# Optimization experiments

Measured on AMD Instinct MI355X. Metric: run time of the kernel, lower is better.

The kernel has to match this reference:

```python
import jax, jax.numpy as jnp
import numpy as np

B, T, D, E, V = 16, 256, 512, 512, 32000  # batch, seqlen, embed_dim, encoder_embed_dim, vocab


def setup_inputs() -> dict:
    key = jax.random.key(0)
    ks = jax.random.split(key, 13)
    s = 0.05
    return {
        "prev_output_tokens": jax.random.randint(ks[0], (B, T), 0, V),
        "encoder_out": jax.random.normal(ks[1], (B, E), jnp.float32),
        "embed": jax.random.normal(ks[2], (V, D), jnp.float32) * s,
        "W_ih0": jax.random.normal(ks[3], (4 * D, E + D), jnp.float32) * s,
        "W_hh0": jax.random.normal(ks[4], (4 * D, D), jnp.float32) * s,
        "b_ih0": jax.random.normal(ks[5], (4 * D,), jnp.float32) * s,
        "b_hh0": jax.random.normal(ks[6], (4 * D,), jnp.float32) * s,
        "W_ih1": jax.random.normal(ks[7], (4 * D, D), jnp.float32) * s,
        "W_hh1": jax.random.normal(ks[8], (4 * D, D), jnp.float32) * s,
        "b_ih1": jax.random.normal(ks[9], (4 * D,), jnp.float32) * s,
        "b_hh1": jax.random.normal(ks[10], (4 * D,), jnp.float32) * s,
        "W_out": jax.random.normal(ks[11], (V, D), jnp.float32) * s,
        "b_out": jax.random.normal(ks[12], (V,), jnp.float32) * s,
    }


def _lstm_cell(x, h, c, W_ih, W_hh, b_ih, b_hh):
    # torch.nn.LSTMCell gate order: i, f, g, o
    gates = x @ W_ih.T + b_ih + h @ W_hh.T + b_hh
    i, f, g, o = jnp.split(gates, 4, axis=-1)
    c_new = jax.nn.sigmoid(f) * c + jax.nn.sigmoid(i) * jnp.tanh(g)
    h_new = jax.nn.sigmoid(o) * jnp.tanh(c_new)
    return h_new, c_new


def reference(prev_output_tokens, encoder_out, embed, W_ih0, W_hh0, b_ih0, b_hh0,
              W_ih1, W_hh1, b_ih1, b_hh1, W_out, b_out):
    # padding_idx=0 -> row 0 of the embedding table is zero
    embed = embed.at[0].set(0.0)
    x = embed[prev_output_tokens]          # [B, T, D]  (dropout: eval mode -> identity)
    x = jnp.swapaxes(x, 0, 1)              # [T, B, D]
    bsz = x.shape[1]
    h0 = jnp.zeros((bsz, W_hh0.shape[1]), x.dtype)
    c0, h1, c1 = h0, h0, h0

    def step(carry, x_t):
        h0, c0, h1, c1 = carry
        inp = jnp.concatenate([x_t, encoder_out], axis=1)   # [B, D+E]
        h0, c0 = _lstm_cell(inp, h0, c0, W_ih0, W_hh0, b_ih0, b_hh0)
        h1, c1 = _lstm_cell(h0, h1, c1, W_ih1, W_hh1, b_ih1, b_hh1)
        return (h0, c0, h1, c1), h1

    _, outs = jax.lax.scan(step, (h0, c0, h1, c1), x)       # outs: [T, B, D]
    outs = jnp.swapaxes(outs, 0, 1)                          # [B, T, D]
    return outs @ W_out.T + b_out                            # [B, T, V]
```

## Files before the change

### kernel.cpp

```cpp
#include <hip/hip_runtime.h>
#include <hip/hip_bf16.h>
#include <math.h>

#define BB 16
#define TT 256
#define DD 512
#define EE 512
#define VV 32000
#define G4 2048

typedef __attribute__((ext_vector_type(4))) float f32x4;
typedef __attribute__((ext_vector_type(8))) short bf16x8;
typedef __attribute__((ext_vector_type(4))) unsigned u32x4;

union lf_u { u32x4 q; bf16x8 v; };

#define SENTMASK32 0x40004000u

__device__ __forceinline__ unsigned short f2bf(float x) {
    unsigned u = __float_as_uint(x);
    unsigned r = (u + 0x7FFFu + ((u >> 16) & 1u)) >> 16;
    return (unsigned short)r;
}

__device__ __forceinline__ float sigmoidf_(float x) { return 1.0f / (1.0f + expf(-x)); }

__global__ __launch_bounds__(256) void k_gather(const int* __restrict__ tok,
        const float* __restrict__ embed, unsigned short* __restrict__ Xb) {
    int m = blockIdx.x;
    int tk = tok[m];
    const float* src = embed + (size_t)tk * DD;
    int i = threadIdx.x * 2;
    float vx = 0.f, vy = 0.f;
    if (tk != 0) { float2 v = *(const float2*)&src[i]; vx = v.x; vy = v.y; }
    ushort2 o; o.x = f2bf(vx); o.y = f2bf(vy);
    *(ushort2*)&Xb[(size_t)m * DD + i] = o;
}

__global__ __launch_bounds__(256) void k_cvt(const float* __restrict__ in,
        unsigned short* __restrict__ out, int n4) {
    int i = blockIdx.x * 256 + threadIdx.x;
    if (i >= n4) return;
    float4 v = ((const float4*)in)[i];
    ushort4 o; o.x = f2bf(v.x); o.y = f2bf(v.y); o.z = f2bf(v.z); o.w = f2bf(v.w);
    ((ushort4*)out)[i] = o;
}

__global__ __launch_bounds__(256) void k_cvt_wih0x(const float* __restrict__ Wih0,
        unsigned short* __restrict__ out) {
    int i = blockIdx.x * 256 + threadIdx.x;
    int j = i >> 7;
    int k4 = (i & 127) << 2;
    float4 v = *(const float4*)&Wih0[(size_t)j * (EE + DD) + k4];
    ushort4 o; o.x = f2bf(v.x); o.y = f2bf(v.y); o.z = f2bf(v.z); o.w = f2bf(v.w);
    *(ushort4*)&out[(size_t)j * DD + k4] = o;
}

__global__ __launch_bounds__(256) void k_encterm(const float* __restrict__ enc,
        const float* __restrict__ Wih0, const float* __restrict__ bih0,
        const float* __restrict__ bhh0, float* __restrict__ et) {
    int b = blockIdx.x >> 3, jc = blockIdx.x & 7;
    int tid = threadIdx.x, lane = tid & 63, w = tid >> 6;
    __shared__ float es[EE];
    if (tid < EE / 4) *(float4*)&es[tid * 4] = *(const float4*)&enc[b * EE + tid * 4];
    __syncthreads();
    float4 e0 = *(const float4*)&es[lane * 4];
    float4 e1 = *(const float4*)&es[256 + lane * 4];
    for (int o = 0; o < 64; ++o) {
        int j = jc * 256 + w * 64 + o;
        const float4* Wr = (const float4*)&Wih0[(size_t)j * (EE + DD) + DD];
        float4 w0 = Wr[lane], w1 = Wr[64 + lane];
        float s = w0.x*e0.x + w0.y*e0.y + w0.z*e0.z + w0.w*e0.w
                + w1.x*e1.x + w1.y*e1.y + w1.z*e1.z + w1.w*e1.w;
        #pragma unroll
        for (int off = 32; off; off >>= 1) s += __shfl_xor(s, off);
        if (lane == 0) et[b * G4 + j] = s + bih0[j] + bhh0[j];
    }
}

template<int EPI>
__global__ __launch_bounds__(256) void k_gemm_bt(
        const unsigned short* __restrict__ A, const unsigned short* __restrict__ Bm,
        float* __restrict__ C, const float* __restrict__ extra,
        int M, int N, int K) {
    __shared__ __align__(16) unsigned short Alds[128 * 32];
    __shared__ __align__(16) unsigned short Blds[128 * 32];
    int tid = threadIdx.x, lane = tid & 63, w = tid >> 6;
    int wr = w >> 1, wc = w & 1;
    int nwgx = gridDim.x;
    int nwg = nwgx * gridDim.y;
    int lin = blockIdx.y * nwgx + blockIdx.x;
    int cpx = nwg >> 3;
    lin = (lin & 7) * cpx + (lin >> 3);
    int m0 = (lin % nwgx) * 128, n0 = (lin / nwgx) * 128;
    f32x4 acc[4][4];
    #pragma unroll
    for (int i = 0; i < 4; i++)
        #pragma unroll
        for (int j = 0; j < 4; j++) acc[i][j] = (f32x4)0.f;

    const char* Abase = (const char*)A;
    const char* Bbase = (const char*)Bm;
    for (int ks = 0; ks < K; ks += 32) {
        #pragma unroll
        for (int c = 0; c < 2; ++c) {
            int f = (tid + c * 256) * 16;
            int row = f >> 6;
            int inb = f & 63;
            const char* gA = Abase + (((size_t)(m0 + row) * K + ks) * 2 + inb);
            __builtin_amdgcn_global_load_lds(
                (const __attribute__((address_space(1))) void*)gA,
                (__attribute__((address_space(3))) void*)((char*)Alds + f), 16, 0, 0);
            const char* gB = Bbase + (((size_t)(n0 + row) * K + ks) * 2 + inb);
            __builtin_amdgcn_global_load_lds(
                (const __attribute__((address_space(1))) void*)gB,
                (__attribute__((address_space(3))) void*)((char*)Blds + f), 16, 0, 0);
        }
        __syncthreads();
        bf16x8 af[4], bfr[4];
        int r = lane & 15, ko = (lane >> 4) * 8;
        #pragma unroll
        for (int mi = 0; mi < 4; ++mi)
            af[mi] = *(const bf16x8*)&Alds[(wr * 64 + mi * 16 + r) * 32 + ko];
        #pragma unroll
        for (int ni = 0; ni < 4; ++ni)
            bfr[ni] = *(const bf16x8*)&Blds[(wc * 64 + ni * 16 + r) * 32 + ko];
        #pragma unroll
        for (int mi = 0; mi < 4; ++mi)
            #pragma unroll
            for (int ni = 0; ni < 4; ++ni)
                acc[mi][ni] = __builtin_amdgcn_mfma_f32_16x16x32_bf16(af[mi], bfr[ni], acc[mi][ni], 0, 0, 0);
        __syncthreads();
    }
    int cr = (lane >> 4) * 4, cc = lane & 15;
    #pragma unroll
    for (int mi = 0; mi < 4; ++mi) {
        #pragma unroll
        for (int ni = 0; ni < 4; ++ni) {
            int col = n0 + wc * 64 + ni * 16 + cc;
            #pragma unroll
            for (int rr = 0; rr < 4; ++rr) {
                int rowg = m0 + wr * 64 + mi * 16 + cr + rr;
                float v = acc[mi][ni][rr];
                if (EPI == 0) v += extra[(rowg >> 8) * G4 + col];
                else          v += extra[col];
                C[(size_t)rowg * N + col] = v;
            }
        }
    }
}

__device__ __forceinline__ void load16sc(const void* base, lf_u* o) {
    asm volatile(
        "global_load_dwordx4 %0, %16, off sc0 sc1\n\t"
        "global_load_dwordx4 %1, %16, off offset:64 sc0 sc1\n\t"
        "global_load_dwordx4 %2, %16, off offset:128 sc0 sc1\n\t"
        "global_load_dwordx4 %3, %16, off offset:192 sc0 sc1\n\t"
        "global_load_dwordx4 %4, %16, off offset:256 sc0 sc1\n\t"
        "global_load_dwordx4 %5, %16, off offset:320 sc0 sc1\n\t"
        "global_load_dwordx4 %6, %16, off offset:384 sc0 sc1\n\t"
        "global_load_dwordx4 %7, %16, off offset:448 sc0 sc1\n\t"
        "global_load_dwordx4 %8, %16, off offset:512 sc0 sc1\n\t"
        "global_load_dwordx4 %9, %16, off offset:576 sc0 sc1\n\t"
        "global_load_dwordx4 %10, %16, off offset:640 sc0 sc1\n\t"
        "global_load_dwordx4 %11, %16, off offset:704 sc0 sc1\n\t"
        "global_load_dwordx4 %12, %16, off offset:768 sc0 sc1\n\t"
        "global_load_dwordx4 %13, %16, off offset:832 sc0 sc1\n\t"
        "global_load_dwordx4 %14, %16, off offset:896 sc0 sc1\n\t"
        "global_load_dwordx4 %15, %16, off offset:960 sc0 sc1\n\t"
        "s_waitcnt vmcnt(0)"
        : "=&v"(o[0].q), "=&v"(o[1].q), "=&v"(o[2].q), "=&v"(o[3].q),
          "=&v"(o[4].q), "=&v"(o[5].q), "=&v"(o[6].q), "=&v"(o[7].q),
          "=&v"(o[8].q), "=&v"(o[9].q), "=&v"(o[10].q), "=&v"(o[11].q),
          "=&v"(o[12].q), "=&v"(o[13].q), "=&v"(o[14].q), "=&v"(o[15].q)
        : "v"(base)
        : "memory");
}

__device__ __forceinline__ void poll16sc(const void* base, lf_u* o) {
    for (;;) {
        load16sc(base, o);
        unsigned bad = 0;
        #pragma unroll
        for (int kt = 0; kt < 16; ++kt)
            bad |= (o[kt].q.x | o[kt].q.y | o[kt].q.z | o[kt].q.w);
        if (!__any((bad & SENTMASK32) != 0)) return;
    }
}

__device__ __forceinline__ void store8sc(void* addr, unsigned long long v) {
    asm volatile("global_store_dwordx2 %0, %1, off sc0 sc1"
                 :: "v"(addr), "v"(v) : "memory");
}

__global__ __launch_bounds__(64) void k_recur(
        const float* __restrict__ Gx,
        const float* __restrict__ Whh0,
        const float* __restrict__ Wih1, const float* __restrict__ Whh1,
        const float* __restrict__ bih1, const float* __restrict__ bhh1,
        unsigned short* h0hist, unsigned short* outsb,
        const unsigned short* zbuf) {
    __shared__ __align__(16) unsigned short wfrag[4 * 32 * 512];
    __shared__ __align__(8)  unsigned short houts[16 * 16];
    const int l = threadIdx.x;
    const int bid = blockIdx.x;
    const int role = bid >> 5;
    const int blk = bid & 31;
    const int d0 = blk * 16;
    const int r16 = l & 15;
    const int q = l >> 4;
    const int ksub = q * 8;
    const int b0 = q * 4;
    const int srow = l >> 2;
    const int sseg = l & 3;

    const int nkt = role ? 32 : 16;
    for (int tile = 0; tile < 4; ++tile) {
        int j = tile * 512 + d0 + r16;
        for (int kt = 0; kt < nkt; ++kt) {
            const float* src;
            if (role == 0)    src = Whh0 + (size_t)j * DD + kt * 32 + ksub;
            else if (kt < 16) src = Wih1 + (size_t)j * DD + kt * 32 + ksub;
            else              src = Whh1 + (size_t)j * DD + (kt - 16) * 32 + ksub;
            float4 x = *(const float4*)src;
            float4 y = *(const float4*)(src + 4);
            bf16x8 w;
            w[0] = f2bf(x.x); w[1] = f2bf(x.y); w[2] = f2bf(x.z); w[3] = f2bf(x.w);
            w[4] = f2bf(y.x); w[5] = f2bf(y.y); w[6] = f2bf(y.z); w[7] = f2bf(y.w);
            *(bf16x8*)&wfrag[((tile * 32 + kt) * 64 + l) * 8] = w;
        }
    }
    __syncthreads();

    float cst[4] = {0.f, 0.f, 0.f, 0.f};
    lf_u xf[16];

    if (role == 0) {
        for (int t = 0; t < TT; ++t) {
            float gx[4][4];
            #pragma unroll
            for (int ni = 0; ni < 4; ++ni)
                #pragma unroll
                for (int rr = 0; rr < 4; ++rr)
                    gx[ni][rr] = Gx[((size_t)(b0 + rr) * TT + t) * G4 + ni * 512 + d0 + r16];

            const char* xb = (const char*)(h0hist + (size_t)t * (BB * DD) + r16 * DD) + q * 16;
            poll16sc(xb, xf);

            f32x4 acc[4];
            #pragma unroll
            for (int ni = 0; ni < 4; ++ni) acc[ni] = (f32x4)0.f;
            #pragma unroll
            for (int kt = 0; kt < 16; ++kt) {
                #pragma unroll
                for (int ni = 0; ni < 4; ++ni) {
                    bf16x8 wf = *(const bf16x8*)&wfrag[((ni * 32 + kt) * 64 + l) * 8];
                    acc[ni] = __builtin_amdgcn_mfma_f32_16x16x32_bf16(xf[kt].v, wf, acc[ni], 0, 0, 0);
                }
            }
            #pragma unroll
            for (int rr = 0; rr < 4; ++rr) {
                float gi = acc[0][rr] + gx[0][rr], gf = acc[1][rr] + gx[1][rr];
                float gg = acc[2][rr] + gx[2][rr], go = acc[3][rr] + gx[3][rr];
                float cn = sigmoidf_(gf) * cst[rr] + sigmoidf_(gi) * tanhf(gg);
                float hn = sigmoidf_(go) * tanhf(cn);
                cst[rr] = cn;
                houts[(b0 + rr) * 16 + r16] = f2bf(hn);
            }
            asm volatile("" ::: "memory");
            {
                const unsigned short* hp = &houts[srow * 16 + sseg * 4];
                unsigned long long w8 =  (unsigned long long)hp[0]
                                      | ((unsigned long long)hp[1] << 16)
                                      | ((unsigned long long)hp[2] << 32)
                                      | ((unsigned long long)hp[3] << 48);
                store8sc(h0hist + (size_t)(t + 1) * (BB * DD) + srow * DD + d0 + sseg * 4, w8);
            }
        }
    } else {
        lf_u hf[16];
        float bin[4];
        #pragma unroll
        for (int ni = 0; ni < 4; ++ni)
            bin[ni] = bih1[ni * 512 + d0 + r16] + bhh1[ni * 512 + d0 + r16];
        for (int t = 0; t < TT; ++t) {
            const char* xb = (const char*)(h0hist + (size_t)(t + 1) * (BB * DD) + r16 * DD) + q * 16;
            poll16sc(xb, xf);

            f32x4 acc[4];
            #pragma unroll
            for (int ni = 0; ni < 4; ++ni)
                acc[ni] = (f32x4){bin[ni], bin[ni], bin[ni], bin[ni]};
            #pragma unroll
            for (int kt = 0; kt < 16; ++kt) {
                #pragma unroll
                for (int ni = 0; ni < 4; ++ni) {
                    bf16x8 wf = *(const bf16x8*)&wfrag[((ni * 32 + kt) * 64 + l) * 8];
                    acc[ni] = __builtin_amdgcn_mfma_f32_16x16x32_bf16(xf[kt].v, wf, acc[ni], 0, 0, 0);
                }
            }
            const char* hb = (t == 0)
                ? (const char*)(zbuf + r16 * DD) + q * 16
                : (const char*)(outsb + ((size_t)r16 * TT + (t - 1)) * DD) + q * 16;
            poll16sc(hb, hf);
            #pragma unroll
            for (int kt = 0; kt < 16; ++kt) {
                #pragma unroll
                for (int ni = 0; ni < 4; ++ni) {
                    bf16x8 wf = *(const bf16x8*)&wfrag[((ni * 32 + 16 + kt) * 64 + l) * 8];
                    acc[ni] = __builtin_amdgcn_mfma_f32_16x16x32_bf16(hf[kt].v, wf, acc[ni], 0, 0, 0);
                }
            }
            #pragma unroll
            for (int rr = 0; rr < 4; ++rr) {
                float gi = acc[0][rr], gf = acc[1][rr], gg = acc[2][rr], go = acc[3][rr];
                float cn = sigmoidf_(gf) * cst[rr] + sigmoidf_(gi) * tanhf(gg);
                float hn = sigmoidf_(go) * tanhf(cn);
                cst[rr] = cn;
                houts[(b0 + rr) * 16 + r16] = f2bf(hn);
            }
            asm volatile("" ::: "memory");
            {
                const unsigned short* hp = &houts[srow * 16 + sseg * 4];
                unsigned long long w8 =  (unsigned long long)hp[0]
                                      | ((unsigned long long)hp[1] << 16)
                                      | ((unsigned long long)hp[2] << 32)
                                      | ((unsigned long long)hp[3] << 48);
                store8sc(outsb + ((size_t)srow * TT + t) * DD + d0 + sseg * 4, w8);
            }
        }
    }
}

extern "C" void kernel_launch(void* const* d_in, const int* in_sizes, int n_in,
                              void* d_out, int out_size, void* d_ws, size_t ws_size,
                              hipStream_t stream) {
    const int*   tok   = (const int*)  d_in[0];
    const float* enc   = (const float*)d_in[1];
    const float* embed = (const float*)d_in[2];
    const float* Wih0  = (const float*)d_in[3];
    const float* Whh0  = (const float*)d_in[4];
    const float* bih0  = (const float*)d_in[5];
    const float* bhh0  = (const float*)d_in[6];
    const float* Wih1  = (const float*)d_in[7];
    const float* Whh1  = (const float*)d_in[8];
    const float* bih1  = (const float*)d_in[9];
    const float* bhh1  = (const float*)d_in[10];
    const float* Wout  = (const float*)d_in[11];
    const float* bout  = (const float*)d_in[12];
    float* out = (float*)d_out;

    char* ws = (char*)d_ws;
    size_t off = 0;
    auto alloc = [&](size_t bytes) -> char* {
        char* p = ws + off; off += (bytes + 255) & ~(size_t)255; return p;
    };
    unsigned short* Xb     = (unsigned short*)alloc((size_t)BB * TT * DD * 2);
    unsigned short* Wih0xb = (unsigned short*)alloc((size_t)G4 * DD * 2);
    unsigned short* Woutb  = (unsigned short*)alloc((size_t)VV * DD * 2);
    float*          et     = (float*)alloc((size_t)BB * G4 * sizeof(float));
    float*          Gx     = (float*)alloc((size_t)BB * TT * G4 * sizeof(float));
    unsigned short* outsb  = (unsigned short*)alloc((size_t)BB * TT * DD * 2);
    unsigned short* h0hist = (unsigned short*)alloc((size_t)(TT + 1) * BB * DD * 2);
    unsigned short* zbuf   = (unsigned short*)alloc((size_t)BB * DD * 2);

    hipMemsetAsync(h0hist, 0, (size_t)BB * DD * 2, stream);
    hipMemsetAsync(h0hist + (size_t)BB * DD, 0xFF, (size_t)TT * BB * DD * 2, stream);
    hipMemsetAsync(outsb, 0xFF, (size_t)BB * TT * DD * 2, stream);
    hipMemsetAsync(zbuf, 0, (size_t)BB * DD * 2, stream);

    k_gather<<<BB * TT, 256, 0, stream>>>(tok, embed, Xb);
    k_cvt<<<(VV * DD / 4 + 255) / 256, 256, 0, stream>>>(Wout, Woutb, VV * DD / 4);
    k_cvt_wih0x<<<(G4 * DD / 4) / 256, 256, 0, stream>>>(Wih0, Wih0xb);
    k_encterm<<<BB * 8, 256, 0, stream>>>(enc, Wih0, bih0, bhh0, et);

    dim3 g1(BB * TT / 128, G4 / 128);
    k_gemm_bt<0><<<g1, 256, 0, stream>>>(Xb, Wih0xb, Gx, et, BB * TT, G4, DD);

    k_recur<<<64, 64, 0, stream>>>(Gx, Whh0, Wih1, Whh1, bih1, bhh1,
                                   h0hist, outsb, zbuf);

    dim3 g2(BB * TT / 128, VV / 128);
    k_gemm_bt<1><<<g2, 256, 0, stream>>>(outsb, Woutb, out, bout, BB * TT, VV, DD);
}
```

Before: 1.677 ms.

## Fuse recurrence and output projection into one persistent kernel with overlap

Merges the LSTM recurrence kernel and the vocab projection GEMM into a single persistent kernel. 64 blocks run the recurrence and publish per-block progress counters after every timestep. The remaining 192 blocks take output GEMM tiles (16 timesteps by 8 batches by 128 vocab columns) from an atomic ticket and spin until the recurrence has produced those timesteps. This overlaps the large projection GEMM with the serial recurrence, at the cost of competing for memory bandwidth, extra polling traffic, and a GEMM tile layout with strided rows.

```diff
diff --git a/kernel.cpp b/kernel.cpp
--- a/kernel.cpp
+++ b/kernel.cpp
@@ -8,6 +8,7 @@
 #define EE 512
 #define VV 32000
 #define G4 2048
+#define NTILES (16 * 2 * 250)
 
 typedef __attribute__((ext_vector_type(4))) float f32x4;
 typedef __attribute__((ext_vector_type(8))) short bf16x8;
@@ -78,8 +79,7 @@
     }
 }
 
-template<int EPI>
-__global__ __launch_bounds__(256) void k_gemm_bt(
+__global__ __launch_bounds__(256) void k_gemm0(
         const unsigned short* __restrict__ A, const unsigned short* __restrict__ Bm,
         float* __restrict__ C, const float* __restrict__ extra,
         int M, int N, int K) {
@@ -141,10 +141,7 @@
             #pragma unroll
             for (int rr = 0; rr < 4; ++rr) {
                 int rowg = m0 + wr * 64 + mi * 16 + cr + rr;
-                float v = acc[mi][ni][rr];
-                if (EPI == 0) v += extra[(rowg >> 8) * G4 + col];
-                else          v += extra[col];
-                C[(size_t)rowg * N + col] = v;
+                C[(size_t)rowg * N + col] = acc[mi][ni][rr] + extra[(rowg >> 8) * G4 + col];
             }
         }
     }
@@ -193,140 +190,242 @@
                  :: "v"(addr), "v"(v) : "memory");
 }
 
-__global__ __launch_bounds__(64) void k_recur(
+__global__ __launch_bounds__(256) void k_mega(
         const float* __restrict__ Gx,
         const float* __restrict__ Whh0,
         const float* __restrict__ Wih1, const float* __restrict__ Whh1,
         const float* __restrict__ bih1, const float* __restrict__ bhh1,
         unsigned short* h0hist, unsigned short* outsb,
-        const unsigned short* zbuf) {
-    __shared__ __align__(16) unsigned short wfrag[4 * 32 * 512];
-    __shared__ __align__(8)  unsigned short houts[16 * 16];
-    const int l = threadIdx.x;
+        const unsigned short* zbuf,
+        const unsigned short* __restrict__ Woutb, const float* __restrict__ bout,
+        float* __restrict__ out,
+        int* ep1, int* tick) {
+    __shared__ __align__(16) unsigned char smem[4 * 32 * 512 * 2 + 512];
+    __shared__ int idSh;
     const int bid = blockIdx.x;
-    const int role = bid >> 5;
-    const int blk = bid & 31;
-    const int d0 = blk * 16;
-    const int r16 = l & 15;
-    const int q = l >> 4;
-    const int ksub = q * 8;
-    const int b0 = q * 4;
-    const int srow = l >> 2;
-    const int sseg = l & 3;
-
-    const int nkt = role ? 32 : 16;
-    for (int tile = 0; tile < 4; ++tile) {
-        int j = tile * 512 + d0 + r16;
-        for (int kt = 0; kt < nkt; ++kt) {
-            const float* src;
-            if (role == 0)    src = Whh0 + (size_t)j * DD + kt * 32 + ksub;
-            else if (kt < 16) src = Wih1 + (size_t)j * DD + kt * 32 + ksub;
-            else              src = Whh1 + (size_t)j * DD + (kt - 16) * 32 + ksub;
-            float4 x = *(const float4*)src;
-            float4 y = *(const float4*)(src + 4);
-            bf16x8 w;
-            w[0] = f2bf(x.x); w[1] = f2bf(x.y); w[2] = f2bf(x.z); w[3] = f2bf(x.w);
-            w[4] = f2bf(y.x); w[5] = f2bf(y.y); w[6] = f2bf(y.z); w[7] = f2bf(y.w);
-            *(bf16x8*)&wfrag[((tile * 32 + kt) * 64 + l) * 8] = w;
+
+    if (bid < 64) {
+        unsigned short* wfrag = (unsigned short*)smem;
+        unsigned short* houts = (unsigned short*)(smem + 4 * 32 * 512 * 2);
+        const int l = threadIdx.x;
+        const int role = bid >> 5;
+        const int blk = bid & 31;
+        const int d0 = blk * 16;
+        const int r16 = l & 15;
+        const int q = (l >> 4) & 3;
+        const int ksub = q * 8;
+        const int b0 = q * 4;
+        const int srow = (l >> 2) & 15;
+        const int sseg = l & 3;
+
+        const int nkt = role ? 32 : 16;
+        if (l < 64) {
+            for (int tile = 0; tile < 4; ++tile) {
+                int j = tile * 512 + d0 + r16;
+                for (int kt = 0; kt < nkt; ++kt) {
+                    const float* src;
+                    if (role == 0)    src = Whh0 + (size_t)j * DD + kt * 32 + ksub;
+                    else if (kt < 16) src = Wih1 + (size_t)j * DD + kt * 32 + ksub;
+                    else              src = Whh1 + (size_t)j * DD + (kt - 16) * 32 + ksub;
+                    float4 x = *(const float4*)src;
+                    float4 y = *(const float4*)(src + 4);
+                    bf16x8 w;
+                    w[0] = f2bf(x.x); w[1] = f2bf(x.y); w[2] = f2bf(x.z); w[3] = f2bf(x.w);
+                    w[4] = f2bf(y.x); w[5] = f2bf(y.y); w[6] = f2bf(y.z); w[7] = f2bf(y.w);
+                    *(bf16x8*)&wfrag[((tile * 32 + kt) * 64 + l) * 8] = w;
+                }
+            }
         }
-    }
-    __syncthreads();
-
-    float cst[4] = {0.f, 0.f, 0.f, 0.f};
-    lf_u xf[16];
-
-    if (role == 0) {
-        for (int t = 0; t < TT; ++t) {
-            float gx[4][4];
+        __syncthreads();
+        if (l >= 64) return;
+
+        float cst[4] = {0.f, 0.f, 0.f, 0.f};
+        lf_u xf[16];
+
+        if (role == 0) {
+            for (int t = 0; t < TT; ++t) {
+                float gx[4][4];
+                #pragma unroll
+                for (int ni = 0; ni < 4; ++ni)
+                    #pragma unroll
+                    for (int rr = 0; rr < 4; ++rr)
+                        gx[ni][rr] = Gx[((size_t)(b0 + rr) * TT + t) * G4 + ni * 512 + d0 + r16];
+
+                const char* xb = (const char*)(h0hist + (size_t)t * (BB * DD) + r16 * DD) + q * 16;
+                poll16sc(xb, xf);
+
+                f32x4 acc[4];
+                #pragma unroll
+                for (int ni = 0; ni < 4; ++ni) acc[ni] = (f32x4)0.f;
+                #pragma unroll
+                for (int kt = 0; kt < 16; ++kt) {
+                    #pragma unroll
+                    for (int ni = 0; ni < 4; ++ni) {
+                        bf16x8 wf = *(const bf16x8*)&wfrag[((ni * 32 + kt) * 64 + l) * 8];
+                        acc[ni] = __builtin_amdgcn_mfma_f32_16x16x32_bf16(xf[kt].v, wf, acc[ni], 0, 0, 0);
+                    }
+                }
+                #pragma unroll
+                for (int rr = 0; rr < 4; ++rr) {
+                    float gi = acc[0][rr] + gx[0][rr], gf = acc[1][rr] + gx[1][rr];
+                    float gg = acc[2][rr] + gx[2][rr], go = acc[3][rr] + gx[3][rr];
+                    float cn = sigmoidf_(gf) * cst[rr] + sigmoidf_(gi) * tanhf(gg);
+                    float hn = sigmoidf_(go) * tanhf(cn);
+                    cst[rr] = cn;
+                    houts[(b0 + rr) * 16 + r16] = f2bf(hn);
+                }
+                asm volatile("" ::: "memory");
+                {
+                    const unsigned short* hp = &houts[srow * 16 + sseg * 4];
+                    unsigned long long w8 =  (unsigned long long)hp[0]
+                                          | ((unsigned long long)hp[1] << 16)
+                                          | ((unsigned long long)hp[2] << 32)
+                                          | ((unsigned long long)hp[3] << 48);
+                    store8sc(h0hist + (size_t)(t + 1) * (BB * DD) + srow * DD + d0 + sseg * 4, w8);
+                }
+            }
+        } else {
+            lf_u hf[16];
+            float bin[4];
             #pragma unroll
             for (int ni = 0; ni < 4; ++ni)
-                #pragma unroll
-                for (int rr = 0; rr < 4; ++rr)
-                    gx[ni][rr] = Gx[((size_t)(b0 + rr) * TT + t) * G4 + ni * 512 + d0 + r16];
-
-            const char* xb = (const char*)(h0hist + (size_t)t * (BB * DD) + r16 * DD) + q * 16;
-            poll16sc(xb, xf);
-
-            f32x4 acc[4];
-            #pragma unroll
-            for (int ni = 0; ni < 4; ++ni) acc[ni] = (f32x4)0.f;
-            #pragma unroll
-            for (int kt = 0; kt < 16; ++kt) {
-                #pragma unroll
-                for (int ni = 0; ni < 4; ++ni) {
-                    bf16x8 wf = *(const bf16x8*)&wfrag[((ni * 32 + kt) * 64 + l) * 8];
-                    acc[ni] = __builtin_amdgcn_mfma_f32_16x16x32_bf16(xf[kt].v, wf, acc[ni], 0, 0, 0);
-                }
-            }
-            #pragma unroll
-            for (int rr = 0; rr < 4; ++rr) {
-                float gi = acc[0][rr] + gx[0][rr], gf = acc[1][rr] + gx[1][rr];
-                float gg = acc[2][rr] + gx[2][rr], go = acc[3][rr] + gx[3][rr];
-                float cn = sigmoidf_(gf) * cst[rr] + sigmoidf_(gi) * tanhf(gg);
-                float hn = sigmoidf_(go) * tanhf(cn);
-                cst[rr] = cn;
-                houts[(b0 + rr) * 16 + r16] = f2bf(hn);
-            }
-            asm volatile("" ::: "memory");
-            {
-                const unsigned short* hp = &houts[srow * 16 + sseg * 4];
-                unsigned long long w8 =  (unsigned long long)hp[0]
-                                      | ((unsigned long long)hp[1] << 16)
-                                      | ((unsigned long long)hp[2] << 32)
-                                      | ((unsigned long long)hp[3] << 48);
-                store8sc(h0hist + (size_t)(t + 1) * (BB * DD) + srow * DD + d0 + sseg * 4, w8);
+                bin[ni] = bih1[ni * 512 + d0 + r16] + bhh1[ni * 512 + d0 + r16];
+            for (int t = 0; t < TT; ++t) {
+                const char* xb = (const char*)(h0hist + (size_t)(t + 1) * (BB * DD) + r16 * DD) + q * 16;
+                poll16sc(xb, xf);
+
+                f32x4 acc[4];
+                #pragma unroll
+                for (int ni = 0; ni < 4; ++ni)
+                    acc[ni] = (f32x4){bin[ni], bin[ni], bin[ni], bin[ni]};
+                #pragma unroll
+                for (int kt = 0; kt < 16; ++kt) {
+                    #pragma unroll
+                    for (int ni = 0; ni < 4; ++ni) {
+                        bf16x8 wf = *(const bf16x8*)&wfrag[((ni * 32 + kt) * 64 + l) * 8];
+                        acc[ni] = __builtin_amdgcn_mfma_f32_16x16x32_bf16(xf[kt].v, wf, acc[ni], 0, 0, 0);
+                    }
+                }
+                const char* hb = (t == 0)
+                    ? (const char*)(zbuf + r16 * DD) + q * 16
+                    : (const char*)(outsb + ((size_t)r16 * TT + (t - 1)) * DD) + q * 16;
+                poll16sc(hb, hf);
+                #pragma unroll
+                for (int kt = 0; kt < 16; ++kt) {
+                    #pragma unroll
+                    for (int ni = 0; ni < 4; ++ni) {
+                        bf16x8 wf = *(const bf16x8*)&wfrag[((ni * 32 + 16 + kt) * 64 + l) * 8];
+                        acc[ni] = __builtin_amdgcn_mfma_f32_16x16x32_bf16(hf[kt].v, wf, acc[ni], 0, 0, 0);
+                    }
+                }
+                #pragma unroll
+                for (int rr = 0; rr < 4; ++rr) {
+                    float gi = acc[0][rr], gf = acc[1][rr], gg = acc[2][rr], go = acc[3][rr];
+                    float cn = sigmoidf_(gf) * cst[rr] + sigmoidf_(gi) * tanhf(gg);
+                    float hn = sigmoidf_(go) * tanhf(cn);
+                    cst[rr] = cn;
+                    houts[(b0 + rr) * 16 + r16] = f2bf(hn);
+                }
+                asm volatile("" ::: "memory");
+                {
+                    const unsigned short* hp = &houts[srow * 16 + sseg * 4];
+                    unsigned long long w8 =  (unsigned long long)hp[0]
+                                          | ((unsigned long long)hp[1] << 16)
+                                          | ((unsigned long long)hp[2] << 32)
+                                          | ((unsigned long long)hp[3] << 48);
+                    store8sc(outsb + ((size_t)srow * TT + t) * DD + d0 + sseg * 4, w8);
+                }
+                asm volatile("s_waitcnt vmcnt(0)" ::: "memory");
+                if (l == 0) {
+                    int tv = t + 1;
+                    asm volatile("global_store_dword %0, %1, off sc0 sc1"
+                                 :: "v"(ep1 + blk * 16), "v"(tv) : "memory");
+                }
             }
         }
     } else {
-        lf_u hf[16];
-        float bin[4];
-        #pragma unroll
-        for (int ni = 0; ni < 4; ++ni)
-            bin[ni] = bih1[ni * 512 + d0 + r16] + bhh1[ni * 512 + d0 + r16];
-        for (int t = 0; t < TT; ++t) {
-            const char* xb = (const char*)(h0hist + (size_t)(t + 1) * (BB * DD) + r16 * DD) + q * 16;
-            poll16sc(xb, xf);
-
-            f32x4 acc[4];
+        unsigned short* Alds = (unsigned short*)smem;
+        unsigned short* Blds = (unsigned short*)(smem + 8192);
+        const int tid = threadIdx.x, lane = tid & 63, w = tid >> 6;
+        const int wr = w >> 1, wc = w & 1;
+
+        for (;;) {
+            if (tid == 0) idSh = atomicAdd(tick, 1);
+            __syncthreads();
+            int id = idSh;
+            if (id >= NTILES) break;
+
+            int chunk = id / 500;
+            int rem   = id % 500;
+            int bg    = rem / 250;
+            int nt    = rem % 250;
+            int t0 = chunk * 16;
+            int n0 = nt * 128;
+            int target = t0 + 16;
+
+            for (;;) {
+                int v;
+                asm volatile("global_load_dword %0, %1, off sc0 sc1\n\ts_waitcnt vmcnt(0)"
+                             : "=v"(v) : "v"(ep1 + (lane & 31) * 16) : "memory");
+                if (__all(v >= target)) break;
+                __builtin_amdgcn_s_sleep(4);
+            }
+
+            f32x4 acc[4][4];
             #pragma unroll
-            for (int ni = 0; ni < 4; ++ni)
-                acc[ni] = (f32x4){bin[ni], bin[ni], bin[ni], bin[ni]};
+            for (int i = 0; i < 4; i++)
+                #pragma unroll
+                for (int j = 0; j < 4; j++) acc[i][j] = (f32x4)0.f;
+
+            for (int ks = 0; ks < DD; ks += 32) {
+                #pragma unroll
+                for (int c = 0; c < 2; ++c) {
+                    int f = (tid + c * 256) * 16;
+                    int row = f >> 6;
+                    int inb = f & 63;
+                    int bb = bg * 8 + (row >> 4);
+                    int tt = t0 + (row & 15);
+                    const char* gA = (const char*)outsb +
+                        (((size_t)bb * TT + tt) * DD + ks) * 2 + inb;
+                    __builtin_amdgcn_global_load_lds(
+                        (const __attribute__((address_space(1))) void*)gA,
+                        (__attribute__((address_space(3))) void*)((char*)Alds + f), 16, 0, 0);
+                    const char* gB = (const char*)Woutb +
+                        (((size_t)(n0 + row)) * DD + ks) * 2 + inb;
+                    __builtin_amdgcn_global_load_lds(
+                        (const __attribute__((address_space(1))) void*)gB,
+                        (__attribute__((address_space(3))) void*)((char*)Blds + f), 16, 0, 0);
+                }
+                __syncthreads();
+                bf16x8 af[4], bfr[4];
+                int r = lane & 15, ko = (lane >> 4) * 8;
+                #pragma unroll
+                for (int mi = 0; mi < 4; ++mi)
+                    af[mi] = *(const bf16x8*)&Alds[(wr * 64 + mi * 16 + r) * 32 + ko];
+                #pragma unroll
+                for (int ni = 0; ni < 4; ++ni)
+                    bfr[ni] = *(const bf16x8*)&Blds[(wc * 64 + ni * 16 + r) * 32 + ko];
+                #pragma unroll
+                for (int mi = 0; mi < 4; ++mi)
+                    #pragma unroll
+                    for (int ni = 0; ni < 4; ++ni)
+                        acc[mi][ni] = __builtin_amdgcn_mfma_f32_16x16x32_bf16(af[mi], bfr[ni], acc[mi][ni], 0, 0, 0);
+                __syncthreads();
+            }
+            int cr = (lane >> 4) * 4, cc = lane & 15;
             #pragma unroll
-            for (int kt = 0; kt < 16; ++kt) {
+            for (int mi = 0; mi < 4; ++mi) {
                 #pragma unroll
                 for (int ni = 0; ni < 4; ++ni) {
-                    bf16x8 wf = *(const bf16x8*)&wfrag[((ni * 32 + kt) * 64 + l) * 8];
-                    acc[ni] = __builtin_amdgcn_mfma_f32_16x16x32_bf16(xf[kt].v, wf, acc[ni], 0, 0, 0);
-                }
-            }
-            const char* hb = (t == 0)
-                ? (const char*)(zbuf + r16 * DD) + q * 16
-                : (const char*)(outsb + ((size_t)r16 * TT + (t - 1)) * DD) + q * 16;
-            poll16sc(hb, hf);
-            #pragma unroll
-            for (int kt = 0; kt < 16; ++kt) {
-                #pragma unroll
-                for (int ni = 0; ni < 4; ++ni) {
-                    bf16x8 wf = *(const bf16x8*)&wfrag[((ni * 32 + 16 + kt) * 64 + l) * 8];
-                    acc[ni] = __builtin_amdgcn_mfma_f32_16x16x32_bf16(hf[kt].v, wf, acc[ni], 0, 0, 0);
-                }
-            }
-            #pragma unroll
-            for (int rr = 0; rr < 4; ++rr) {
-                float gi = acc[0][rr], gf = acc[1][rr], gg = acc[2][rr], go = acc[3][rr];
-                float cn = sigmoidf_(gf) * cst[rr] + sigmoidf_(gi) * tanhf(gg);
-                float hn = sigmoidf_(go) * tanhf(cn);
-                cst[rr] = cn;
-                houts[(b0 + rr) * 16 + r16] = f2bf(hn);
-            }
-            asm volatile("" ::: "memory");
-            {
-                const unsigned short* hp = &houts[srow * 16 + sseg * 4];
-                unsigned long long w8 =  (unsigned long long)hp[0]
-                                      | ((unsigned long long)hp[1] << 16)
-                                      | ((unsigned long long)hp[2] << 32)
-                                      | ((unsigned long long)hp[3] << 48);
-                store8sc(outsb + ((size_t)srow * TT + t) * DD + d0 + sseg * 4, w8);
+                    int col = n0 + wc * 64 + ni * 16 + cc;
+                    #pragma unroll
+                    for (int rr = 0; rr < 4; ++rr) {
+                        int rloc = wr * 64 + mi * 16 + cr + rr;
+                        int bb = bg * 8 + (rloc >> 4);
+                        int tt = t0 + (rloc & 15);
+                        out[((size_t)bb * TT + tt) * VV + col] = acc[mi][ni][rr] + bout[col];
+                    }
+                }
             }
         }
     }
@@ -363,11 +462,15 @@
     unsigned short* outsb  = (unsigned short*)alloc((size_t)BB * TT * DD * 2);
     unsigned short* h0hist = (unsigned short*)alloc((size_t)(TT + 1) * BB * DD * 2);
     unsigned short* zbuf   = (unsigned short*)alloc((size_t)BB * DD * 2);
+    int*            ep1    = (int*)alloc(32 * 16 * sizeof(int));
+    int*            tick   = (int*)alloc(64 * sizeof(int));
 
     hipMemsetAsync(h0hist, 0, (size_t)BB * DD * 2, stream);
     hipMemsetAsync(h0hist + (size_t)BB * DD, 0xFF, (size_t)TT * BB * DD * 2, stream);
     hipMemsetAsync(outsb, 0xFF, (size_t)BB * TT * DD * 2, stream);
     hipMemsetAsync(zbuf, 0, (size_t)BB * DD * 2, stream);
+    hipMemsetAsync(ep1, 0, 32 * 16 * sizeof(int), stream);
+    hipMemsetAsync(tick, 0, 64 * sizeof(int), stream);
 
     k_gather<<<BB * TT, 256, 0, stream>>>(tok, embed, Xb);
     k_cvt<<<(VV * DD / 4 + 255) / 256, 256, 0, stream>>>(Wout, Woutb, VV * DD / 4);
@@ -375,11 +478,9 @@
     k_encterm<<<BB * 8, 256, 0, stream>>>(enc, Wih0, bih0, bhh0, et);
 
     dim3 g1(BB * TT / 128, G4 / 128);
-    k_gemm_bt<0><<<g1, 256, 0, stream>>>(Xb, Wih0xb, Gx, et, BB * TT, G4, DD);
-
-    k_recur<<<64, 64, 0, stream>>>(Gx, Whh0, Wih1, Whh1, bih1, bhh1,
-                                   h0hist, outsb, zbuf);
-
-    dim3 g2(BB * TT / 128, VV / 128);
-    k_gemm_bt<1><<<g2, 256, 0, stream>>>(outsb, Woutb, out, bout, BB * TT, VV, DD);
-}
+    k_gemm0<<<g1, 256, 0, stream>>>(Xb, Wih0xb, Gx, et, BB * TT, G4, DD);
+
+    k_mega<<<256, 256, 0, stream>>>(Gx, Whh0, Wih1, Whh1, bih1, bhh1,
+                                    h0hist, outsb, zbuf,
+                                    Woutb, bout, out, ep1, tick);
+}
```

Result: faster. 1.592 ms (-5.1%).
